# Kernel tuning notes

Hardware: AMD Instinct MI355X
Metric: run time of the kernel (lower is better)

The kernel has to match this reference:

```python
import jax, jax.numpy as jnp
import numpy as np

B, C_IN, L = 8, 64, 4096
C_OUT, HEADS = 64, 3
E = 524288
T_DIM = 256
N = B * L
EPS = 1e-5
NEG_SLOPE = 0.2  # PyG GATConv default negative_slope


def setup_inputs() -> dict:
    key = jax.random.key(0)
    ks = jax.random.split(key, 12)
    x = jax.random.normal(ks[0], (B, C_IN, L), jnp.float32)
    time_emb = jax.random.normal(ks[1], (B, T_DIM), jnp.float32)
    edge_index = jax.random.randint(ks[2], (2, E), 0, N, dtype=jnp.int32)
    # GATConv params: lin maps in -> heads*out; att_src/att_dst per head
    W_lin = jax.random.normal(ks[3], (C_IN, HEADS * C_OUT), jnp.float32) / np.sqrt(C_IN)
    att_src = jax.random.normal(ks[4], (1, HEADS, C_OUT), jnp.float32) / np.sqrt(C_OUT)
    att_dst = jax.random.normal(ks[5], (1, HEADS, C_OUT), jnp.float32) / np.sqrt(C_OUT)
    bias = jnp.zeros((C_OUT,), jnp.float32)
    # time projection (computed but unused in the source forward)
    tp_W = jax.random.normal(ks[6], (T_DIM, C_OUT), jnp.float32) / np.sqrt(T_DIM)
    tp_b = jnp.zeros((C_OUT,), jnp.float32)
    # BatchNorm1d affine params (training-mode batch stats)
    gamma = jnp.ones((C_OUT,), jnp.float32)
    beta = jnp.zeros((C_OUT,), jnp.float32)
    return {"x": x, "time_emb": time_emb, "edge_index": edge_index,
            "W_lin": W_lin, "att_src": att_src, "att_dst": att_dst,
            "bias": bias, "tp_W": tp_W, "tp_b": tp_b,
            "gamma": gamma, "beta": beta}


def reference(x, time_emb, edge_index, W_lin, att_src, att_dst, bias, tp_W, tp_b, gamma, beta):
    b, c, l = x.shape
    n = b * l
    # time projection: present in source but its result is never used
    _t = (time_emb @ tp_W + tp_b)[:, :, None]  # [b, C_OUT, 1] (dead)
    h = (x.reshape(-1, c) @ W_lin).reshape(n, HEADS, C_OUT)  # [N,H,C]
    a_src = (h * att_src).sum(-1)  # [N,H]
    a_dst = (h * att_dst).sum(-1)  # [N,H]
    # add self loops (PyG default add_self_loops=True)
    loops = jnp.arange(n, dtype=edge_index.dtype)
    src = jnp.concatenate([edge_index[0], loops])
    dst = jnp.concatenate([edge_index[1], loops])
    e = a_src[src] + a_dst[dst]                        # [E+N, H]
    e = jnp.where(e > 0, e, NEG_SLOPE * e)             # LeakyReLU
    emax = jax.ops.segment_max(e, dst, num_segments=n)  # every node has a self loop
    ex = jnp.exp(e - emax[dst])
    denom = jax.ops.segment_sum(ex, dst, num_segments=n)
    alpha = ex / denom[dst]                            # segment softmax over dst
    msg = alpha[:, :, None] * h[src]                   # [E+N, H, C]
    out = jax.ops.segment_sum(msg, dst, num_segments=n)  # [N,H,C]
    out = out.mean(axis=1) + bias                      # concat=False -> head mean
    # BatchNorm1d (training mode: biased batch stats)
    mu = out.mean(axis=0)
    var = ((out - mu) ** 2).mean(axis=0)
    out = (out - mu) / jnp.sqrt(var + EPS) * gamma + beta
    out = jax.nn.relu(out)
    return out.reshape(b, -1, l)
```

## Files before the change

### kernel.cpp

```cpp
#include <hip/hip_runtime.h>
#include <hip/hip_bf16.h>

#define N_NODES 32768
#define E_EDGES 524288
#define HC 192
#define NEG_SLOPE 0.2f
#define BN_EPS 1e-5f
#define PAD 64

typedef _Float16 f16;

#define FUSED_BLOCKS 2048
#define GEMM_WAVES (1536 * 4)

__device__ __forceinline__ float lrelu(float v) { return v > 0.f ? v : NEG_SLOPE * v; }

__device__ __forceinline__ float wave_sum(float v) {
#pragma unroll
    for (int off = 32; off > 0; off >>= 1) v += __shfl_xor(v, off);
    return v;
}
__device__ __forceinline__ float rlane(float v, int l) {
    return __uint_as_float(__builtin_amdgcn_readlane(__float_as_uint(v), l));
}

__global__ __launch_bounds__(256, 2) void k_fused(
        const int4* __restrict__ src4, const int4* __restrict__ dst4,
        int* __restrict__ cnt, unsigned short* __restrict__ csr_pad,
        const float* __restrict__ x, const float* __restrict__ W,
        const float* __restrict__ att_s, const float* __restrict__ att_d,
        f16* __restrict__ hh, float* __restrict__ a_src, float* __restrict__ a_dst,
        float* __restrict__ gp1, float* __restrict__ gp2) {
    if ((blockIdx.x & 3) == 0) {
        int i = (blockIdx.x >> 2) * 256 + threadIdx.x;
        int4 s = src4[i];
        int4 d = dst4[i];
        int p0 = atomicAdd(&cnt[d.x], 1);
        int p1 = atomicAdd(&cnt[d.y], 1);
        int p2 = atomicAdd(&cnt[d.z], 1);
        int p3 = atomicAdd(&cnt[d.w], 1);
        if (p0 < PAD) csr_pad[d.x * PAD + p0] = (unsigned short)s.x;
        if (p1 < PAD) csr_pad[d.y * PAD + p1] = (unsigned short)s.y;
        if (p2 < PAD) csr_pad[d.z * PAD + p2] = (unsigned short)s.z;
        if (p3 < PAD) csr_pad[d.w * PAD + p3] = (unsigned short)s.w;
        if (blockIdx.x == 0) {
            float4 z = make_float4(0.f, 0.f, 0.f, 0.f);
#pragma unroll
            for (int i2 = 0; i2 < 4; i2++) {
                ((float4*)gp1)[threadIdx.x * 4 + i2] = z;
                ((float4*)gp2)[threadIdx.x * 4 + i2] = z;
            }
        }
        return;
    }
    const int gbid  = blockIdx.x - (blockIdx.x >> 2) - 1;
    const int lane  = threadIdx.x & 63;
    const int wid   = (gbid * 256 + threadIdx.x) >> 6;
    const int head  = wid / (GEMM_WAVES / 3);
    const int wslot = wid % (GEMM_WAVES / 3);
    const int c     = head * 64 + lane;

    float wcol[64];
#pragma unroll
    for (int k = 0; k < 64; k++) wcol[k] = W[k * HC + c];
    const float As = att_s[c];
    const float Ad = att_d[c];

#pragma unroll 1
    for (int n = wslot; n < N_NODES; n += (GEMM_WAVES / 3)) {
        float xv = x[(size_t)n * 64 + lane];
        float acc = 0.f;
#pragma unroll
        for (int k = 0; k < 64; k++) {
            float xk = rlane(xv, k);
            acc = fmaf(xk, wcol[k], acc);
        }
        hh[(size_t)n * HC + c] = (f16)acc;
        float s = wave_sum(acc * As);
        float d = wave_sum(acc * Ad);
        if (lane == 0) {
            a_src[n * 4 + head] = s;
            a_dst[n * 4 + head] = d;
        }
    }
}

__global__ __launch_bounds__(256, 4) void k_node(
        const f16* __restrict__ hh,
        const float* __restrict__ a_src,
        const float* __restrict__ a_dst,
        const int* __restrict__ cnt,
        const unsigned short* __restrict__ csr_pad,
        const float* __restrict__ bias,
        float* __restrict__ out_pre,
        float* __restrict__ gp1,
        float* __restrict__ gp2) {
    const int lane = threadIdx.x & 63;
    const int wv = threadIdx.x >> 6;
    const int n = blockIdx.x * 4 + wv;

    int deg = cnt[n]; if (deg > PAD) deg = PAD;
    const unsigned short* __restrict__ row = csr_pad + n * PAD;

    const float ad0 = a_dst[n * 4 + 0], ad1 = a_dst[n * 4 + 1], ad2 = a_dst[n * 4 + 2];

    float ws0 = __expf(lrelu(a_src[n * 4 + 0] + ad0));
    float ws1 = __expf(lrelu(a_src[n * 4 + 1] + ad1));
    float ws2 = __expf(lrelu(a_src[n * 4 + 2] + ad2));
    float den0 = ws0, den1 = ws1, den2 = ws2;
    const f16* hn = hh + (size_t)n * HC;
    float acc0 = ws0 * (float)hn[lane];
    float acc1 = ws1 * (float)hn[64 + lane];
    float acc2 = ws2 * (float)hn[128 + lane];

    int s = 0;
    float w0 = 0.f, w1 = 0.f, w2 = 0.f;
    if (lane < deg) {
        s = (int)row[lane];
        float4 as = ((const float4*)a_src)[s];
        w0 = __expf(lrelu(as.x + ad0));
        w1 = __expf(lrelu(as.y + ad1));
        w2 = __expf(lrelu(as.z + ad2));
    }
    den0 += wave_sum(w0);
    den1 += wave_sum(w1);
    den2 += wave_sum(w2);

    int j = 0;
    for (; j + 8 <= deg; j += 8) {
#pragma unroll
        for (int u = 0; u < 8; u += 4) {
            int s0 = __builtin_amdgcn_readlane(s, j + u);
            int s1 = __builtin_amdgcn_readlane(s, j + u + 1);
            int s2 = __builtin_amdgcn_readlane(s, j + u + 2);
            int s3 = __builtin_amdgcn_readlane(s, j + u + 3);
            const f16* __restrict__ h0 = hh + (size_t)s0 * HC;
            const f16* __restrict__ h1 = hh + (size_t)s1 * HC;
            const f16* __restrict__ h2 = hh + (size_t)s2 * HC;
            const f16* __restrict__ h3 = hh + (size_t)s3 * HC;
            float v00 = (float)h0[lane], v01 = (float)h0[64 + lane], v02 = (float)h0[128 + lane];
            float v10 = (float)h1[lane], v11 = (float)h1[64 + lane], v12 = (float)h1[128 + lane];
            float v20 = (float)h2[lane], v21 = (float)h2[64 + lane], v22 = (float)h2[128 + lane];
            float v30 = (float)h3[lane], v31 = (float)h3[64 + lane], v32 = (float)h3[128 + lane];
            float w00 = rlane(w0, j + u),     w01 = rlane(w1, j + u),     w02 = rlane(w2, j + u);
            float w10 = rlane(w0, j + u + 1), w11 = rlane(w1, j + u + 1), w12 = rlane(w2, j + u + 1);
            float w20 = rlane(w0, j + u + 2), w21 = rlane(w1, j + u + 2), w22 = rlane(w2, j + u + 2);
            float w30 = rlane(w0, j + u + 3), w31 = rlane(w1, j + u + 3), w32 = rlane(w2, j + u + 3);
            acc0 = fmaf(w00, v00, acc0); acc0 = fmaf(w10, v10, acc0);
            acc0 = fmaf(w20, v20, acc0); acc0 = fmaf(w30, v30, acc0);
            acc1 = fmaf(w01, v01, acc1); acc1 = fmaf(w11, v11, acc1);
            acc1 = fmaf(w21, v21, acc1); acc1 = fmaf(w31, v31, acc1);
            acc2 = fmaf(w02, v02, acc2); acc2 = fmaf(w12, v12, acc2);
            acc2 = fmaf(w22, v22, acc2); acc2 = fmaf(w32, v32, acc2);
        }
    }
    for (; j < deg; j++) {
        int sa = __builtin_amdgcn_readlane(s, j);
        const f16* __restrict__ ha = hh + (size_t)sa * HC;
        float wa0 = rlane(w0, j), wa1 = rlane(w1, j), wa2 = rlane(w2, j);
        acc0 = fmaf(wa0, (float)ha[lane], acc0);
        acc1 = fmaf(wa1, (float)ha[64 + lane], acc1);
        acc2 = fmaf(wa2, (float)ha[128 + lane], acc2);
    }

    float outv = (acc0 / den0 + acc1 / den1 + acc2 / den2) * (1.0f / 3.0f) + bias[lane];
    out_pre[n * 64 + lane] = outv;

    __shared__ float ls[4][64], lq[4][64];
    ls[wv][lane] = outv;
    lq[wv][lane] = outv * outv;
    __syncthreads();
    if (threadIdx.x < 64) {
        int t = threadIdx.x;
        float s_ = ls[0][t] + ls[1][t] + ls[2][t] + ls[3][t];
        float q_ = lq[0][t] + lq[1][t] + lq[2][t] + lq[3][t];
        int slice = blockIdx.x & 63;
        atomicAdd(&gp1[slice * 64 + t], s_);
        atomicAdd(&gp2[slice * 64 + t], q_);
    }
}

#define APPLY_BLOCKS 512
__global__ __launch_bounds__(256) void k_apply(const float4* __restrict__ out_pre4,
                                               const float* __restrict__ gp1,
                                               const float* __restrict__ gp2,
                                               const float* __restrict__ gamma,
                                               const float* __restrict__ beta,
                                               float4* __restrict__ out4) {
    __shared__ float sc[64], sh[64];
    if (threadIdx.x < 64) {
        int t = threadIdx.x;
        float s = 0.f, q = 0.f;
        for (int i = 0; i < 64; i++) { s += gp1[i * 64 + t]; q += gp2[i * 64 + t]; }
        const float inv_n = 1.0f / (float)N_NODES;
        float mu = s * inv_n;
        float var = q * inv_n - mu * mu;
        float invstd = 1.0f / sqrtf(var + BN_EPS);
        float scale = invstd * gamma[t];
        sc[t] = scale;
        sh[t] = beta[t] - mu * scale;
    }
    __syncthreads();
    const int total = N_NODES * 64 / 4;
    for (int idx = blockIdx.x * 256 + threadIdx.x; idx < total; idx += APPLY_BLOCKS * 256) {
        int c0 = (idx * 4) & 63;
        float4 v = out_pre4[idx];
        float4 r;
        r.x = fmaxf(v.x * sc[c0 + 0] + sh[c0 + 0], 0.f);
        r.y = fmaxf(v.y * sc[c0 + 1] + sh[c0 + 1], 0.f);
        r.z = fmaxf(v.z * sc[c0 + 2] + sh[c0 + 2], 0.f);
        r.w = fmaxf(v.w * sc[c0 + 3] + sh[c0 + 3], 0.f);
        out4[idx] = r;
    }
}

extern "C" void kernel_launch(void* const* d_in, const int* in_sizes, int n_in,
                              void* d_out, int out_size, void* d_ws, size_t ws_size,
                              hipStream_t stream) {
    const float* x     = (const float*)d_in[0];
    const int*   ei    = (const int*)d_in[2];
    const float* W     = (const float*)d_in[3];
    const float* att_s = (const float*)d_in[4];
    const float* att_d = (const float*)d_in[5];
    const float* bias  = (const float*)d_in[6];
    const float* gamma = (const float*)d_in[9];
    const float* beta  = (const float*)d_in[10];
    float* out = (float*)d_out;

    char* ws = (char*)d_ws;
    size_t off = 0;
    auto alloc = [&](size_t bytes) -> void* {
        void* p = ws + off;
        off += (bytes + 255) & ~(size_t)255;
        return p;
    };
    f16*            hh      = (f16*)alloc((size_t)N_NODES * HC * 2);
    float*          a_src   = (float*)alloc((size_t)N_NODES * 4 * 4);
    float*          a_dst   = (float*)alloc((size_t)N_NODES * 4 * 4);
    int*            cnt     = (int*)alloc((size_t)N_NODES * 4);
    unsigned short* csr_pad = (unsigned short*)alloc((size_t)N_NODES * PAD * 2);
    float*          out_pre = (float*)alloc((size_t)N_NODES * 64 * 4);
    float*          gp1     = (float*)alloc(64 * 64 * 4);
    float*          gp2     = (float*)alloc(64 * 64 * 4);

    hipMemsetAsync(cnt, 0, (size_t)N_NODES * 4, stream);

    k_fused<<<FUSED_BLOCKS, 256, 0, stream>>>((const int4*)ei,
                                              (const int4*)(ei + E_EDGES),
                                              cnt, csr_pad,
                                              x, W, att_s, att_d, hh, a_src, a_dst,
                                              gp1, gp2);
    k_node<<<N_NODES / 4, 256, 0, stream>>>(hh, a_src, a_dst, cnt, csr_pad, bias,
                                            out_pre, gp1, gp2);
    k_apply<<<APPLY_BLOCKS, 256, 0, stream>>>((const float4*)out_pre, gp1, gp2,
                                              gamma, beta, (float4*)out);
}
```

Before: 161.6 us.

## Compute node projection GEMM with MFMA f16 tiles instead of scalar FMA

Replaces the per-wave scalar readlane/FMA projection of x by W with 16x16x32 f16 MFMA instructions, so each wave computes a 16-node by 192-channel tile. Attention logits come from partial dot products reduced with lane shuffles. The scatter and GEMM blocks are now split contiguously (512 each) instead of interleaved. Inputs x and W are rounded to f16 before the multiply, which adds precision loss compared with the fp32 accumulation used before.

```diff
diff --git a/kernel.cpp b/kernel.cpp
--- a/kernel.cpp
+++ b/kernel.cpp
@@ -9,9 +9,11 @@
 #define PAD 64
 
 typedef _Float16 f16;
-
-#define FUSED_BLOCKS 2048
-#define GEMM_WAVES (1536 * 4)
+typedef __attribute__((ext_vector_type(8))) _Float16 v8h;
+typedef __attribute__((ext_vector_type(4))) float    v4f;
+
+#define SCAT_BLOCKS 512
+#define GEMM_BLOCKS 512
 
 __device__ __forceinline__ float lrelu(float v) { return v > 0.f ? v : NEG_SLOPE * v; }
 
@@ -31,8 +33,8 @@
         const float* __restrict__ att_s, const float* __restrict__ att_d,
         f16* __restrict__ hh, float* __restrict__ a_src, float* __restrict__ a_dst,
         float* __restrict__ gp1, float* __restrict__ gp2) {
-    if ((blockIdx.x & 3) == 0) {
-        int i = (blockIdx.x >> 2) * 256 + threadIdx.x;
+    if (blockIdx.x < SCAT_BLOCKS) {
+        int i = blockIdx.x * 256 + threadIdx.x;
         int4 s = src4[i];
         int4 d = dst4[i];
         int p0 = atomicAdd(&cnt[d.x], 1);
@@ -53,34 +55,60 @@
         }
         return;
     }
-    const int gbid  = blockIdx.x - (blockIdx.x >> 2) - 1;
-    const int lane  = threadIdx.x & 63;
-    const int wid   = (gbid * 256 + threadIdx.x) >> 6;
-    const int head  = wid / (GEMM_WAVES / 3);
-    const int wslot = wid % (GEMM_WAVES / 3);
-    const int c     = head * 64 + lane;
-
-    float wcol[64];
-#pragma unroll
-    for (int k = 0; k < 64; k++) wcol[k] = W[k * HC + c];
-    const float As = att_s[c];
-    const float Ad = att_d[c];
-
-#pragma unroll 1
-    for (int n = wslot; n < N_NODES; n += (GEMM_WAVES / 3)) {
-        float xv = x[(size_t)n * 64 + lane];
-        float acc = 0.f;
-#pragma unroll
-        for (int k = 0; k < 64; k++) {
-            float xk = rlane(xv, k);
-            acc = fmaf(xk, wcol[k], acc);
-        }
-        hh[(size_t)n * HC + c] = (f16)acc;
-        float s = wave_sum(acc * As);
-        float d = wave_sum(acc * Ad);
-        if (lane == 0) {
-            a_src[n * 4 + head] = s;
-            a_dst[n * 4 + head] = d;
+    const int lane = threadIdx.x & 63;
+    const int wid  = ((blockIdx.x - SCAT_BLOCKS) * 256 + threadIdx.x) >> 6;
+    const int q    = lane >> 4;
+    const int nl   = lane & 15;
+    const int n0   = wid * 16;
+
+    v8h xf0, xf1;
+    {
+        const float* xr = x + (size_t)(n0 + nl) * 64 + q * 8;
+        float4 lo = *(const float4*)(xr);
+        float4 hi = *(const float4*)(xr + 4);
+        xf0[0] = (f16)lo.x; xf0[1] = (f16)lo.y; xf0[2] = (f16)lo.z; xf0[3] = (f16)lo.w;
+        xf0[4] = (f16)hi.x; xf0[5] = (f16)hi.y; xf0[6] = (f16)hi.z; xf0[7] = (f16)hi.w;
+        lo = *(const float4*)(xr + 32);
+        hi = *(const float4*)(xr + 36);
+        xf1[0] = (f16)lo.x; xf1[1] = (f16)lo.y; xf1[2] = (f16)lo.z; xf1[3] = (f16)lo.w;
+        xf1[4] = (f16)hi.x; xf1[5] = (f16)hi.y; xf1[6] = (f16)hi.z; xf1[7] = (f16)hi.w;
+    }
+
+    float sAcc = 0.f, dAcc = 0.f;
+#pragma unroll
+    for (int ct = 0; ct < 12; ct++) {
+        const int c = ct * 16 + nl;
+        v8h wf0, wf1;
+#pragma unroll
+        for (int j = 0; j < 8; j++) {
+            wf0[j] = (f16)W[(q * 8 + j) * HC + c];
+            wf1[j] = (f16)W[(32 + q * 8 + j) * HC + c];
+        }
+        float4 av = *(const float4*)(att_s + ct * 16 + q * 4);
+        float4 dv = *(const float4*)(att_d + ct * 16 + q * 4);
+
+        v4f C = {0.f, 0.f, 0.f, 0.f};
+        C = __builtin_amdgcn_mfma_f32_16x16x32_f16(wf0, xf0, C, 0, 0, 0);
+        C = __builtin_amdgcn_mfma_f32_16x16x32_f16(wf1, xf1, C, 0, 0, 0);
+
+        union { f16 h[4]; unsigned long long u; } pk;
+        pk.h[0] = (f16)C[0]; pk.h[1] = (f16)C[1];
+        pk.h[2] = (f16)C[2]; pk.h[3] = (f16)C[3];
+        *(unsigned long long*)(hh + (size_t)(n0 + nl) * HC + ct * 16 + q * 4) = pk.u;
+
+        sAcc = fmaf(C[0], av.x, sAcc); sAcc = fmaf(C[1], av.y, sAcc);
+        sAcc = fmaf(C[2], av.z, sAcc); sAcc = fmaf(C[3], av.w, sAcc);
+        dAcc = fmaf(C[0], dv.x, dAcc); dAcc = fmaf(C[1], dv.y, dAcc);
+        dAcc = fmaf(C[2], dv.z, dAcc); dAcc = fmaf(C[3], dv.w, dAcc);
+
+        if ((ct & 3) == 3) {
+            float s = sAcc; s += __shfl_xor(s, 16); s += __shfl_xor(s, 32);
+            float d = dAcc; d += __shfl_xor(d, 16); d += __shfl_xor(d, 32);
+            if (lane < 16) {
+                a_src[(n0 + lane) * 4 + (ct >> 2)] = s;
+                a_dst[(n0 + lane) * 4 + (ct >> 2)] = d;
+            }
+            sAcc = 0.f; dAcc = 0.f;
         }
     }
 }
@@ -245,11 +273,9 @@
 
     hipMemsetAsync(cnt, 0, (size_t)N_NODES * 4, stream);
 
-    k_fused<<<FUSED_BLOCKS, 256, 0, stream>>>((const int4*)ei,
-                                              (const int4*)(ei + E_EDGES),
-                                              cnt, csr_pad,
-                                              x, W, att_s, att_d, hh, a_src, a_dst,
-                                              gp1, gp2);
+    k_fused<<<SCAT_BLOCKS + GEMM_BLOCKS, 256, 0, stream>>>(
+        (const int4*)ei, (const int4*)(ei + E_EDGES), cnt, csr_pad,
+        x, W, att_s, att_d, hh, a_src, a_dst, gp1, gp2);
     k_node<<<N_NODES / 4, 256, 0, stream>>>(hh, a_src, a_dst, cnt, csr_pad, bias,
                                             out_pre, gp1, gp2);
     k_apply<<<APPLY_BLOCKS, 256, 0, stream>>>((const float4*)out_pre, gp1, gp2,
```

Result: faster. 153.0 us (-5.3%).
